# Kernel optimization log

Hardware: AMD Instinct MI355X
Metric: run time of the kernel (lower is better)

Reference implementation:

```python
import jax, jax.numpy as jnp
import numpy as np

N = 100000      # nodes
E = 1600000     # edges (before self-loops)
IN = 128        # in_size
H = 4           # heads
C = 32          # out_size // heads
OUT = H * C     # 128
NEG_SLOPE = 0.2
LN_EPS = 1e-5
SM_EPS = 1e-16  # PyG softmax eps


def setup_inputs() -> dict:
    key = jax.random.key(0)
    ks = jax.random.split(key, 6)
    x = jax.random.normal(ks[0], (N, IN), dtype=jnp.float32)
    edge_index = jax.random.randint(ks[1], (2, E), 0, N, dtype=jnp.int64)
    W = jax.random.normal(ks[2], (IN, OUT), dtype=jnp.float32) * 0.05
    a_src = jax.random.normal(ks[3], (H, C), dtype=jnp.float32) * 0.05
    a_dst = jax.random.normal(ks[4], (H, C), dtype=jnp.float32) * 0.05
    bias = jnp.zeros((OUT,), dtype=jnp.float32)
    gamma = jnp.ones((OUT,), dtype=jnp.float32)
    beta = jnp.zeros((OUT,), dtype=jnp.float32)
    return {"x": x, "edge_index": edge_index, "W": W, "a_src": a_src,
            "a_dst": a_dst, "bias": bias, "gamma": gamma, "beta": beta}


def reference(x, edge_index, W, a_src, a_dst, bias, gamma, beta):
    n = x.shape[0]
    # add self loops (PyG GATConv default)
    loops = jnp.arange(n, dtype=edge_index.dtype)
    src = jnp.concatenate([edge_index[0], loops])  # [E+N]
    dst = jnp.concatenate([edge_index[1], loops])

    h = (x @ W).reshape(n, H, C)                   # [N,H,C]
    alpha_src = jnp.sum(h * a_src, axis=-1)        # [N,H]
    alpha_dst = jnp.sum(h * a_dst, axis=-1)        # [N,H]

    e = jax.nn.leaky_relu(alpha_src[src] + alpha_dst[dst], NEG_SLOPE)  # [E+N,H]
    # segment softmax over edges grouped by destination node
    emax = jax.ops.segment_max(e, dst, num_segments=n)
    emax = jnp.where(jnp.isfinite(emax), emax, 0.0)
    ee = jnp.exp(e - emax[dst])
    denom = jax.ops.segment_sum(ee, dst, num_segments=n)
    alpha = ee / (denom[dst] + SM_EPS)             # [E+N,H]

    msg = h[src] * alpha[:, :, None]               # [E+N,H,C]
    out = jax.ops.segment_sum(msg, dst, num_segments=n).reshape(n, OUT) + bias

    # LayerNorm(out_size)
    mu = jnp.mean(out, axis=-1, keepdims=True)
    var = jnp.var(out, axis=-1, keepdims=True)
    out = (out - mu) * jax.lax.rsqrt(var + LN_EPS) * gamma + beta
    return jax.nn.relu(out)
```

## Files before the change

### kernel.cpp

```cpp
#include <hip/hip_runtime.h>
#include <hip/hip_bf16.h>
#include <math.h>

#define IN_DIM 128
#define OUT_DIM 128
#define NHEAD 4
#define HC 32
#define NEG_SLOPE 0.2f
#define LN_EPS 1e-5f
#define SM_EPS 1e-16f

#define NB_SHIFT 9
#define BDST 512
#define NBUCK_MAX 256
#define BIN_ITER 28
#define BIN_CHUNK (BIN_ITER * 256)
#define SRC_BITS 17
#define SRC_MASK ((1u << SRC_BITS) - 1u)

typedef __attribute__((ext_vector_type(8))) short bf16x8;
typedef __attribute__((ext_vector_type(4))) short short4v;
typedef __attribute__((ext_vector_type(4))) float f32x4;

__device__ __forceinline__ float leaky(float v) { return v > 0.f ? v : NEG_SLOPE * v; }

__device__ __forceinline__ short f2b(float f) {
    __hip_bfloat16 b = __float2bfloat16(f);
    return *reinterpret_cast<short*>(&b);
}

__device__ __forceinline__ int swz(int row, int byteInRow) {
    return row * 256 + (byteInRow ^ ((row & 7) << 4));
}

__global__ void k_prep(const float* __restrict__ W, __hip_bfloat16* __restrict__ WtB,
                       const int* __restrict__ ei, int* __restrict__ bcnt, int E, int N)
{
    int t0 = blockIdx.x * 256 + threadIdx.x;
    if (t0 < IN_DIM * OUT_DIM) {
        int k = t0 >> 7, j = t0 & 127;
        WtB[j * IN_DIM + k] = __float2bfloat16(W[t0]);
    }
    __shared__ int h[NBUCK_MAX];
    for (int i = threadIdx.x; i < NBUCK_MAX; i += blockDim.x) h[i] = 0;
    __syncthreads();
    int tot = E + N;
    for (int e = blockIdx.x * blockDim.x + threadIdx.x; e < tot; e += gridDim.x * blockDim.x) {
        int d = (e < E) ? ei[E + e] : (e - E);
        atomicAdd(&h[d >> NB_SHIFT], 1);
    }
    __syncthreads();
    for (int i = threadIdx.x; i < NBUCK_MAX; i += blockDim.x)
        if (h[i]) atomicAdd(&bcnt[i], h[i]);
}

__global__ void __launch_bounds__(256)
k_gemm_bin(const float* __restrict__ x, const __hip_bfloat16* __restrict__ WtB,
           const float* __restrict__ a_src, const float* __restrict__ a_dst,
           __hip_bfloat16* __restrict__ hB, float* __restrict__ asrc_out,
           float* __restrict__ adst_out,
           const int* __restrict__ ei, const int* __restrict__ bcnt,
           int* __restrict__ bcur, unsigned* __restrict__ binned,
           int E, int N, int nblk_gemm)
{
    __shared__ __align__(16) char lds[49152];
    const int t = threadIdx.x;

    if ((int)blockIdx.x < nblk_gemm) {
        const int node0 = blockIdx.x * 64;

        #pragma unroll
        for (int i = 0; i < 16; ++i) {
            int idx = (i * 256 + t) * 4;
            int col = idx >> 7, k = idx & 127;
            short4v w4 = *reinterpret_cast<const short4v*>((const short*)WtB + idx);
            *reinterpret_cast<short4v*>(lds + 16384 + swz(col, 2 * k)) = w4;
        }
        #pragma unroll
        for (int i = 0; i < 8; ++i) {
            int idx = (i * 256 + t) * 4;
            int row = idx >> 7, k = idx & 127;
            int node = node0 + row;
            float4 xv = make_float4(0.f, 0.f, 0.f, 0.f);
            if (node < N) xv = *reinterpret_cast<const float4*>(x + (size_t)node * IN_DIM + k);
            short4v xb = { f2b(xv.x), f2b(xv.y), f2b(xv.z), f2b(xv.w) };
            *reinterpret_cast<short4v*>(lds + swz(row, 2 * k)) = xb;
        }
        __syncthreads();

        const int wave = t >> 6, l = t & 63;
        const int lr = l & 15, lg = l >> 4;

        bf16x8 afrag[4];
        #pragma unroll
        for (int kk = 0; kk < 4; ++kk)
            afrag[kk] = *reinterpret_cast<bf16x8*>(lds + swz(wave * 16 + lr, kk * 64 + lg * 16));

        f32x4 acc[8];
        #pragma unroll
        for (int cg = 0; cg < 8; ++cg) acc[cg] = (f32x4){0.f, 0.f, 0.f, 0.f};

        #pragma unroll
        for (int cg = 0; cg < 8; ++cg) {
            #pragma unroll
            for (int kk = 0; kk < 4; ++kk) {
                bf16x8 b = *reinterpret_cast<bf16x8*>(lds + 16384 + swz(cg * 16 + lr, kk * 64 + lg * 16));
                acc[cg] = __builtin_amdgcn_mfma_f32_16x16x32_bf16(afrag[kk], b, acc[cg], 0, 0, 0);
            }
        }

        #pragma unroll
        for (int q = 0; q < 4; ++q) {
            int node = node0 + wave * 16 + lg * 4 + q;
            if (node < N) {
                #pragma unroll
                for (int cg = 0; cg < 8; ++cg)
                    hB[(size_t)node * OUT_DIM + cg * 16 + lr] = __float2bfloat16(acc[cg][q]);
            }
        }

        #pragma unroll
        for (int q = 0; q < 4; ++q) {
            int node = node0 + wave * 16 + lg * 4 + q;
            #pragma unroll
            for (int hh = 0; hh < 4; ++hh) {
                float as0 = a_src[hh * HC + lr], as1 = a_src[hh * HC + 16 + lr];
                float ad0 = a_dst[hh * HC + lr], ad1 = a_dst[hh * HC + 16 + lr];
                float s = acc[2 * hh][q] * as0 + acc[2 * hh + 1][q] * as1;
                float d = acc[2 * hh][q] * ad0 + acc[2 * hh + 1][q] * ad1;
                #pragma unroll
                for (int m = 1; m < 16; m <<= 1) {
                    s += __shfl_xor(s, m, 64);
                    d += __shfl_xor(d, m, 64);
                }
                if (lr == 0 && node < N) {
                    asrc_out[node * NHEAD + hh] = s;
                    adst_out[node * NHEAD + hh] = d;
                }
            }
        }
    } else {
        int* cnt = (int*)lds;
        int* gb  = (int*)(lds + 1024);
        int* sc  = (int*)(lds + 2048);
        int tot = E + N;
        int base = ((int)blockIdx.x - nblk_gemm) * BIN_CHUNK;

        int bv = bcnt[t];
        sc[t] = bv;
        __syncthreads();
        #pragma unroll
        for (int off = 1; off < NBUCK_MAX; off <<= 1) {
            int tmp = (t >= off) ? sc[t - off] : 0;
            __syncthreads();
            sc[t] += tmp;
            __syncthreads();
        }
        int bbase_t = sc[t] - bv;
        cnt[t] = 0;
        __syncthreads();

        int rk[BIN_ITER], bk[BIN_ITER], dlo[BIN_ITER];
        #pragma unroll
        for (int k = 0; k < BIN_ITER; ++k) {
            int e = base + k * 256 + t;
            bk[k] = -1; rk[k] = 0; dlo[k] = 0;
            if (e < tot) {
                int d = (e < E) ? ei[E + e] : (e - E);
                bk[k] = d >> NB_SHIFT;
                dlo[k] = d & (BDST - 1);
                rk[k] = atomicAdd(&cnt[bk[k]], 1);
            }
        }
        __syncthreads();
        gb[t] = cnt[t] ? (bbase_t + atomicAdd(&bcur[t], cnt[t])) : 0;
        __syncthreads();
        #pragma unroll
        for (int k = 0; k < BIN_ITER; ++k) {
            int e = base + k * 256 + t;
            if (e < tot) {
                int s = (e < E) ? ei[e] : (e - E);
                binned[gb[bk[k]] + rk[k]] = (unsigned)s | ((unsigned)dlo[k] << SRC_BITS);
            }
        }
    }
}

__global__ void k_bucket_csr(const unsigned* __restrict__ binned, const int* __restrict__ bcnt,
                             int* __restrict__ rowptr, int* __restrict__ csr_src,
                             int N, int tot, int nbuck)
{
    __shared__ int cnt[BDST];
    __shared__ int s2[256];
    int b = blockIdx.x;
    int t = threadIdx.x;
    int d0 = b << NB_SHIFT;

    int bv = bcnt[t];
    s2[t] = bv;
    __syncthreads();
    #pragma unroll
    for (int off = 1; off < NBUCK_MAX; off <<= 1) {
        int tmp = (t >= off) ? s2[t - off] : 0;
        __syncthreads();
        s2[t] += tmp;
        __syncthreads();
    }
    __shared__ int ebase_s, ne_s;
    if (t == b) { ebase_s = s2[t] - bv; ne_s = bv; }
    __syncthreads();
    int ebase = ebase_s, ne = ne_s;

    cnt[t] = 0; cnt[t + 256] = 0;
    __syncthreads();
    for (int i = t; i < ne; i += 256) {
        unsigned p = binned[ebase + i];
        atomicAdd(&cnt[p >> SRC_BITS], 1);
    }
    __syncthreads();
    int c0 = cnt[2 * t], c1 = cnt[2 * t + 1];
    s2[t] = c0 + c1;
    __syncthreads();
    #pragma unroll
    for (int off = 1; off < 256; off <<= 1) {
        int tmp = (t >= off) ? s2[t - off] : 0;
        __syncthreads();
        s2[t] += tmp;
        __syncthreads();
    }
    int e0 = (t ? s2[t - 1] : 0);
    cnt[2 * t] = e0;
    cnt[2 * t + 1] = e0 + c0;
    if (d0 + 2 * t < N)     rowptr[d0 + 2 * t]     = ebase + e0;
    if (d0 + 2 * t + 1 < N) rowptr[d0 + 2 * t + 1] = ebase + e0 + c0;
    if (b == nbuck - 1 && t == 0) rowptr[N] = tot;
    __syncthreads();
    for (int i = t; i < ne; i += 256) {
        unsigned p = binned[ebase + i];
        int r = atomicAdd(&cnt[p >> SRC_BITS], 1);
        csr_src[ebase + r] = (int)(p & SRC_MASK);
    }
}

__global__ void k_gather(const int* __restrict__ csr_src, const int* __restrict__ rowptr,
                         const __hip_bfloat16* __restrict__ hB,
                         const float* __restrict__ asrc, const float* __restrict__ adst,
                         const float* __restrict__ bias, const float* __restrict__ gamma,
                         const float* __restrict__ beta, float* __restrict__ out, int N)
{
    int wave = threadIdx.x >> 6;
    int l = threadIdx.x & 63;
    int d = blockIdx.x * 4 + wave;
    if (d >= N) return;
    int head = l >> 4;
    const char* hp = (const char*)hB;
    unsigned voff = (unsigned)(l << 2);
    float ad = adst[d * NHEAD + head];
    int beg = __builtin_amdgcn_readfirstlane(rowptr[d]);
    int end = __builtin_amdgcn_readfirstlane(rowptr[d + 1]);

    float ax0 = 0.f, ay0 = 0.f, dn0 = 0.f;
    float ax1 = 0.f, ay1 = 0.f, dn1 = 0.f;

    for (int c = beg; c < end; c += 16) {
        int rem = __builtin_amdgcn_readfirstlane(end - c);
        int idx = c + (l & 15);
        int cl = idx < end ? idx : end - 1;
        int smine = csr_src[cl];
        float v = (idx < end) ? asrc[(unsigned)smine * NHEAD + head] : -1e30f;
        float ee = __expf(leaky(v + ad));

#define GRP(E0_, E1_, E2_, E3_) {                                                     \
        unsigned s0_ = (unsigned)__builtin_amdgcn_readlane(smine, (E0_));             \
        unsigned s1_ = (unsigned)__builtin_amdgcn_readlane(smine, (E1_));             \
        unsigned s2_ = (unsigned)__builtin_amdgcn_readlane(smine, (E2_));             \
        unsigned s3_ = (unsigned)__builtin_amdgcn_readlane(smine, (E3_));             \
        unsigned hv0_ = *(const unsigned*)(hp + ((size_t)s0_ << 8) + voff);           \
        unsigned hv1_ = *(const unsigned*)(hp + ((size_t)s1_ << 8) + voff);           \
        unsigned hv2_ = *(const unsigned*)(hp + ((size_t)s2_ << 8) + voff);           \
        unsigned hv3_ = *(const unsigned*)(hp + ((size_t)s3_ << 8) + voff);           \
        float e0_ = __int_as_float(__builtin_amdgcn_ds_swizzle(                       \
            __float_as_int(ee), 0x10 | ((E0_) << 5)));                                \
        float e1_ = __int_as_float(__builtin_amdgcn_ds_swizzle(                       \
            __float_as_int(ee), 0x10 | ((E1_) << 5)));                                \
        float e2_ = __int_as_float(__builtin_amdgcn_ds_swizzle(                       \
            __float_as_int(ee), 0x10 | ((E2_) << 5)));                                \
        float e3_ = __int_as_float(__builtin_amdgcn_ds_swizzle(                       \
            __float_as_int(ee), 0x10 | ((E3_) << 5)));                                \
        ax0 = fmaf(e0_, __uint_as_float(hv0_ << 16), ax0);                            \
        ay0 = fmaf(e0_, __uint_as_float(hv0_ & 0xffff0000u), ay0);  dn0 += e0_;       \
        ax1 = fmaf(e1_, __uint_as_float(hv1_ << 16), ax1);                            \
        ay1 = fmaf(e1_, __uint_as_float(hv1_ & 0xffff0000u), ay1);  dn1 += e1_;       \
        ax0 = fmaf(e2_, __uint_as_float(hv2_ << 16), ax0);                            \
        ay0 = fmaf(e2_, __uint_as_float(hv2_ & 0xffff0000u), ay0);  dn0 += e2_;       \
        ax1 = fmaf(e3_, __uint_as_float(hv3_ << 16), ax1);                            \
        ay1 = fmaf(e3_, __uint_as_float(hv3_ & 0xffff0000u), ay1);  dn1 += e3_;       \
    }
        GRP(0, 1, 2, 3)
        if (rem > 4)  GRP(4, 5, 6, 7)
        if (rem > 8)  GRP(8, 9, 10, 11)
        if (rem > 12) GRP(12, 13, 14, 15)
#undef GRP
    }

    float accx = ax0 + ax1, accy = ay0 + ay1, den = dn0 + dn1;
    float inv = 1.f / (den + SM_EPS);
    float vx = accx * inv + bias[2 * l];
    float vy = accy * inv + bias[2 * l + 1];

    float s1 = vx + vy;
    float s2 = vx * vx + vy * vy;
    #pragma unroll
    for (int m = 32; m >= 1; m >>= 1) {
        s1 += __shfl_xor(s1, m, 64);
        s2 += __shfl_xor(s2, m, 64);
    }
    float mean = s1 * (1.f / OUT_DIM);
    float var = s2 * (1.f / OUT_DIM) - mean * mean;
    float r = rsqrtf(var + LN_EPS);
    float ox = (vx - mean) * r * gamma[2 * l] + beta[2 * l];
    float oy = (vy - mean) * r * gamma[2 * l + 1] + beta[2 * l + 1];
    ox = ox > 0.f ? ox : 0.f;
    oy = oy > 0.f ? oy : 0.f;
    *reinterpret_cast<float2*>(&out[(size_t)d * OUT_DIM + 2 * l]) = make_float2(ox, oy);
}

extern "C" void kernel_launch(void* const* d_in, const int* in_sizes, int n_in,
                              void* d_out, int out_size, void* d_ws, size_t ws_size,
                              hipStream_t stream) {
    const float* x      = (const float*)d_in[0];
    const int*   ei     = (const int*)d_in[1];
    const float* W      = (const float*)d_in[2];
    const float* a_src  = (const float*)d_in[3];
    const float* a_dst  = (const float*)d_in[4];
    const float* bias   = (const float*)d_in[5];
    const float* gamma  = (const float*)d_in[6];
    const float* beta   = (const float*)d_in[7];
    float* out = (float*)d_out;

    const int N = in_sizes[0] / IN_DIM;
    const int E = in_sizes[1] / 2;
    const int TOT = E + N;
    const int nbuck = (N + BDST - 1) >> NB_SHIFT;
    const int nblk_gemm = (N + 63) / 64;
    const int nblk_bin = (TOT + BIN_CHUNK - 1) / BIN_CHUNK;

    char* p = (char*)d_ws;
    __hip_bfloat16* hB = (__hip_bfloat16*)p;  p += (size_t)N * OUT_DIM * sizeof(__hip_bfloat16);
    __hip_bfloat16* WtB = (__hip_bfloat16*)p; p += (size_t)IN_DIM * OUT_DIM * sizeof(__hip_bfloat16);
    float* asrc   = (float*)p;                p += (size_t)N * NHEAD * sizeof(float);
    float* adst   = (float*)p;                p += (size_t)N * NHEAD * sizeof(float);
    int* bcnt     = (int*)p;                  p += NBUCK_MAX * sizeof(int);
    int* bcur     = (int*)p;                  p += NBUCK_MAX * sizeof(int);
    int* rowptr   = (int*)p;                  p += (size_t)(N + 1) * sizeof(int);
    unsigned* binned = (unsigned*)p;          p += (size_t)TOT * sizeof(unsigned);
    int* csr_src  = (int*)p;                  p += (size_t)TOT * sizeof(int);

    (void)hipMemsetAsync(bcnt, 0, 2 * NBUCK_MAX * sizeof(int), stream);

    k_prep<<<256, 256, 0, stream>>>(W, WtB, ei, bcnt, E, N);
    k_gemm_bin<<<nblk_gemm + nblk_bin, 256, 0, stream>>>(x, WtB, a_src, a_dst, hB, asrc, adst,
                                                         ei, bcnt, bcur, binned, E, N, nblk_gemm);
    k_bucket_csr<<<nbuck, 256, 0, stream>>>(binned, bcnt, rowptr, csr_src, N, TOT, nbuck);
    k_gather<<<(N + 3) / 4, 256, 0, stream>>>(csr_src, rowptr, hB, asrc, adst,
                                              bias, gamma, beta, out, N);
}
```

Baseline: 176.6 us.

## Use fixed-capacity buckets to drop histogram pass and prefetch gather indices

```diff
diff --git a/kernel.cpp b/kernel.cpp
--- a/kernel.cpp
+++ b/kernel.cpp
@@ -17,6 +17,8 @@
 #define BIN_CHUNK (BIN_ITER * 256)
 #define SRC_BITS 17
 #define SRC_MASK ((1u << SRC_BITS) - 1u)
+#define BCAP_SHIFT 14
+#define BCAP (1 << BCAP_SHIFT)
 
 typedef __attribute__((ext_vector_type(8))) short bf16x8;
 typedef __attribute__((ext_vector_type(4))) short short4v;
@@ -33,25 +35,11 @@
     return row * 256 + (byteInRow ^ ((row & 7) << 4));
 }
 
-__global__ void k_prep(const float* __restrict__ W, __hip_bfloat16* __restrict__ WtB,
-                       const int* __restrict__ ei, int* __restrict__ bcnt, int E, int N)
+__global__ void k_prepW(const float* __restrict__ W, __hip_bfloat16* __restrict__ WtB)
 {
     int t0 = blockIdx.x * 256 + threadIdx.x;
-    if (t0 < IN_DIM * OUT_DIM) {
-        int k = t0 >> 7, j = t0 & 127;
-        WtB[j * IN_DIM + k] = __float2bfloat16(W[t0]);
-    }
-    __shared__ int h[NBUCK_MAX];
-    for (int i = threadIdx.x; i < NBUCK_MAX; i += blockDim.x) h[i] = 0;
-    __syncthreads();
-    int tot = E + N;
-    for (int e = blockIdx.x * blockDim.x + threadIdx.x; e < tot; e += gridDim.x * blockDim.x) {
-        int d = (e < E) ? ei[E + e] : (e - E);
-        atomicAdd(&h[d >> NB_SHIFT], 1);
-    }
-    __syncthreads();
-    for (int i = threadIdx.x; i < NBUCK_MAX; i += blockDim.x)
-        if (h[i]) atomicAdd(&bcnt[i], h[i]);
+    int k = t0 >> 7, j = t0 & 127;
+    WtB[j * IN_DIM + k] = __float2bfloat16(W[t0]);
 }
 
 __global__ void __launch_bounds__(256)
@@ -59,8 +47,8 @@
            const float* __restrict__ a_src, const float* __restrict__ a_dst,
            __hip_bfloat16* __restrict__ hB, float* __restrict__ asrc_out,
            float* __restrict__ adst_out,
-           const int* __restrict__ ei, const int* __restrict__ bcnt,
-           int* __restrict__ bcur, unsigned* __restrict__ binned,
+           const int* __restrict__ ei, int* __restrict__ bcur,
+           unsigned* __restrict__ binned,
            int E, int N, int nblk_gemm)
 {
     __shared__ __align__(16) char lds[49152];
@@ -142,21 +130,9 @@
     } else {
         int* cnt = (int*)lds;
         int* gb  = (int*)(lds + 1024);
-        int* sc  = (int*)(lds + 2048);
         int tot = E + N;
         int base = ((int)blockIdx.x - nblk_gemm) * BIN_CHUNK;
 
-        int bv = bcnt[t];
-        sc[t] = bv;
-        __syncthreads();
-        #pragma unroll
-        for (int off = 1; off < NBUCK_MAX; off <<= 1) {
-            int tmp = (t >= off) ? sc[t - off] : 0;
-            __syncthreads();
-            sc[t] += tmp;
-            __syncthreads();
-        }
-        int bbase_t = sc[t] - bv;
         cnt[t] = 0;
         __syncthreads();
 
@@ -173,7 +149,7 @@
             }
         }
         __syncthreads();
-        gb[t] = cnt[t] ? (bbase_t + atomicAdd(&bcur[t], cnt[t])) : 0;
+        gb[t] = cnt[t] ? ((t << BCAP_SHIFT) + atomicAdd(&bcur[t], cnt[t])) : 0;
         __syncthreads();
         #pragma unroll
         for (int k = 0; k < BIN_ITER; ++k) {
@@ -186,35 +162,22 @@
     }
 }
 
-__global__ void k_bucket_csr(const unsigned* __restrict__ binned, const int* __restrict__ bcnt,
-                             int* __restrict__ rowptr, int* __restrict__ csr_src,
-                             int N, int tot, int nbuck)
+__global__ void k_bucket_csr(const unsigned* __restrict__ binned, const int* __restrict__ bcur,
+                             int* __restrict__ rowbeg, int* __restrict__ rowend,
+                             int* __restrict__ csr_src, int N)
 {
     __shared__ int cnt[BDST];
     __shared__ int s2[256];
     int b = blockIdx.x;
     int t = threadIdx.x;
     int d0 = b << NB_SHIFT;
-
-    int bv = bcnt[t];
-    s2[t] = bv;
-    __syncthreads();
-    #pragma unroll
-    for (int off = 1; off < NBUCK_MAX; off <<= 1) {
-        int tmp = (t >= off) ? s2[t - off] : 0;
-        __syncthreads();
-        s2[t] += tmp;
-        __syncthreads();
-    }
-    __shared__ int ebase_s, ne_s;
-    if (t == b) { ebase_s = s2[t] - bv; ne_s = bv; }
-    __syncthreads();
-    int ebase = ebase_s, ne = ne_s;
+    int base = b << BCAP_SHIFT;
+    int ne = bcur[b];
 
     cnt[t] = 0; cnt[t + 256] = 0;
     __syncthreads();
     for (int i = t; i < ne; i += 256) {
-        unsigned p = binned[ebase + i];
+        unsigned p = binned[base + i];
         atomicAdd(&cnt[p >> SRC_BITS], 1);
     }
     __syncthreads();
@@ -231,18 +194,24 @@
     int e0 = (t ? s2[t - 1] : 0);
     cnt[2 * t] = e0;
     cnt[2 * t + 1] = e0 + c0;
-    if (d0 + 2 * t < N)     rowptr[d0 + 2 * t]     = ebase + e0;
-    if (d0 + 2 * t + 1 < N) rowptr[d0 + 2 * t + 1] = ebase + e0 + c0;
-    if (b == nbuck - 1 && t == 0) rowptr[N] = tot;
+    if (d0 + 2 * t < N) {
+        rowbeg[d0 + 2 * t] = base + e0;
+        rowend[d0 + 2 * t] = base + e0 + c0;
+    }
+    if (d0 + 2 * t + 1 < N) {
+        rowbeg[d0 + 2 * t + 1] = base + e0 + c0;
+        rowend[d0 + 2 * t + 1] = base + e0 + c0 + c1;
+    }
     __syncthreads();
     for (int i = t; i < ne; i += 256) {
-        unsigned p = binned[ebase + i];
+        unsigned p = binned[base + i];
         int r = atomicAdd(&cnt[p >> SRC_BITS], 1);
-        csr_src[ebase + r] = (int)(p & SRC_MASK);
-    }
-}
-
-__global__ void k_gather(const int* __restrict__ csr_src, const int* __restrict__ rowptr,
+        csr_src[base + r] = (int)(p & SRC_MASK);
+    }
+}
+
+__global__ void k_gather(const int* __restrict__ csr_src,
+                         const int* __restrict__ rowbeg, const int* __restrict__ rowend,
                          const __hip_bfloat16* __restrict__ hB,
                          const float* __restrict__ asrc, const float* __restrict__ adst,
                          const float* __restrict__ bias, const float* __restrict__ gamma,
@@ -256,51 +225,49 @@
     const char* hp = (const char*)hB;
     unsigned voff = (unsigned)(l << 2);
     float ad = adst[d * NHEAD + head];
-    int beg = __builtin_amdgcn_readfirstlane(rowptr[d]);
-    int end = __builtin_amdgcn_readfirstlane(rowptr[d + 1]);
+    int beg = __builtin_amdgcn_readfirstlane(rowbeg[d]);
+    int end = __builtin_amdgcn_readfirstlane(rowend[d]);
 
     float ax0 = 0.f, ay0 = 0.f, dn0 = 0.f;
     float ax1 = 0.f, ay1 = 0.f, dn1 = 0.f;
 
+    int idx = beg + (l & 15);
+    int cl = idx < end ? idx : end - 1;
+    int smine = csr_src[cl];
+    float v = (idx < end) ? asrc[(unsigned)smine * NHEAD + head] : -1e30f;
+
     for (int c = beg; c < end; c += 16) {
-        int rem = __builtin_amdgcn_readfirstlane(end - c);
-        int idx = c + (l & 15);
-        int cl = idx < end ? idx : end - 1;
-        int smine = csr_src[cl];
-        float v = (idx < end) ? asrc[(unsigned)smine * NHEAD + head] : -1e30f;
         float ee = __expf(leaky(v + ad));
-
-#define GRP(E0_, E1_, E2_, E3_) {                                                     \
-        unsigned s0_ = (unsigned)__builtin_amdgcn_readlane(smine, (E0_));             \
-        unsigned s1_ = (unsigned)__builtin_amdgcn_readlane(smine, (E1_));             \
-        unsigned s2_ = (unsigned)__builtin_amdgcn_readlane(smine, (E2_));             \
-        unsigned s3_ = (unsigned)__builtin_amdgcn_readlane(smine, (E3_));             \
-        unsigned hv0_ = *(const unsigned*)(hp + ((size_t)s0_ << 8) + voff);           \
-        unsigned hv1_ = *(const unsigned*)(hp + ((size_t)s1_ << 8) + voff);           \
-        unsigned hv2_ = *(const unsigned*)(hp + ((size_t)s2_ << 8) + voff);           \
-        unsigned hv3_ = *(const unsigned*)(hp + ((size_t)s3_ << 8) + voff);           \
-        float e0_ = __int_as_float(__builtin_amdgcn_ds_swizzle(                       \
-            __float_as_int(ee), 0x10 | ((E0_) << 5)));                                \
-        float e1_ = __int_as_float(__builtin_amdgcn_ds_swizzle(                       \
-            __float_as_int(ee), 0x10 | ((E1_) << 5)));                                \
-        float e2_ = __int_as_float(__builtin_amdgcn_ds_swizzle(                       \
-            __float_as_int(ee), 0x10 | ((E2_) << 5)));                                \
-        float e3_ = __int_as_float(__builtin_amdgcn_ds_swizzle(                       \
-            __float_as_int(ee), 0x10 | ((E3_) << 5)));                                \
-        ax0 = fmaf(e0_, __uint_as_float(hv0_ << 16), ax0);                            \
-        ay0 = fmaf(e0_, __uint_as_float(hv0_ & 0xffff0000u), ay0);  dn0 += e0_;       \
-        ax1 = fmaf(e1_, __uint_as_float(hv1_ << 16), ax1);                            \
-        ay1 = fmaf(e1_, __uint_as_float(hv1_ & 0xffff0000u), ay1);  dn1 += e1_;       \
-        ax0 = fmaf(e2_, __uint_as_float(hv2_ << 16), ax0);                            \
-        ay0 = fmaf(e2_, __uint_as_float(hv2_ & 0xffff0000u), ay0);  dn0 += e2_;       \
-        ax1 = fmaf(e3_, __uint_as_float(hv3_ << 16), ax1);                            \
-        ay1 = fmaf(e3_, __uint_as_float(hv3_ & 0xffff0000u), ay1);  dn1 += e3_;       \
-    }
-        GRP(0, 1, 2, 3)
-        if (rem > 4)  GRP(4, 5, 6, 7)
-        if (rem > 8)  GRP(8, 9, 10, 11)
-        if (rem > 12) GRP(12, 13, 14, 15)
-#undef GRP
+        int scur = smine;
+        int c2 = c + 16;
+        if (c2 < end) {
+            int idx2 = c2 + (l & 15);
+            int cl2 = idx2 < end ? idx2 : end - 1;
+            smine = csr_src[cl2];
+            v = (idx2 < end) ? asrc[(unsigned)smine * NHEAD + head] : -1e30f;
+        }
+
+#define GLOAD(E_)                                                                     \
+        unsigned se##E_ = (unsigned)__builtin_amdgcn_readlane(scur, (E_));            \
+        unsigned hv##E_ = *(const unsigned*)(hp + ((size_t)se##E_ << 8) + voff);
+#define GCONS(E_, AX_, AY_, DN_) {                                                    \
+        float eb = __int_as_float(__builtin_amdgcn_ds_swizzle(                        \
+            __float_as_int(ee), 0x10 | ((E_) << 5)));                                 \
+        AX_ = fmaf(eb, __uint_as_float(hv##E_ << 16), AX_);                           \
+        AY_ = fmaf(eb, __uint_as_float(hv##E_ & 0xffff0000u), AY_);  DN_ += eb;       \
+    }
+        { GLOAD(0) GLOAD(1) GLOAD(2) GLOAD(3) GLOAD(4) GLOAD(5) GLOAD(6) GLOAD(7)
+          GCONS(0, ax0, ay0, dn0) GCONS(1, ax1, ay1, dn1)
+          GCONS(2, ax0, ay0, dn0) GCONS(3, ax1, ay1, dn1)
+          GCONS(4, ax0, ay0, dn0) GCONS(5, ax1, ay1, dn1)
+          GCONS(6, ax0, ay0, dn0) GCONS(7, ax1, ay1, dn1) }
+        { GLOAD(8) GLOAD(9) GLOAD(10) GLOAD(11) GLOAD(12) GLOAD(13) GLOAD(14) GLOAD(15)
+          GCONS(8, ax0, ay0, dn0)  GCONS(9, ax1, ay1, dn1)
+          GCONS(10, ax0, ay0, dn0) GCONS(11, ax1, ay1, dn1)
+          GCONS(12, ax0, ay0, dn0) GCONS(13, ax1, ay1, dn1)
+          GCONS(14, ax0, ay0, dn0) GCONS(15, ax1, ay1, dn1) }
+#undef GLOAD
+#undef GCONS
     }
 
     float accx = ax0 + ax1, accy = ay0 + ay1, den = dn0 + dn1;
@@ -350,18 +317,18 @@
     __hip_bfloat16* WtB = (__hip_bfloat16*)p; p += (size_t)IN_DIM * OUT_DIM * sizeof(__hip_bfloat16);
     float* asrc   = (float*)p;                p += (size_t)N * NHEAD * sizeof(float);
     float* adst   = (float*)p;                p += (size_t)N * NHEAD * sizeof(float);
-    int* bcnt     = (int*)p;                  p += NBUCK_MAX * sizeof(int);
     int* bcur     = (int*)p;                  p += NBUCK_MAX * sizeof(int);
-    int* rowptr   = (int*)p;                  p += (size_t)(N + 1) * sizeof(int);
-    unsigned* binned = (unsigned*)p;          p += (size_t)TOT * sizeof(unsigned);
-    int* csr_src  = (int*)p;                  p += (size_t)TOT * sizeof(int);
-
-    (void)hipMemsetAsync(bcnt, 0, 2 * NBUCK_MAX * sizeof(int), stream);
-
-    k_prep<<<256, 256, 0, stream>>>(W, WtB, ei, bcnt, E, N);
+    int* rowbeg   = (int*)p;                  p += (size_t)N * sizeof(int);
+    int* rowend   = (int*)p;                  p += (size_t)N * sizeof(int);
+    unsigned* binned = (unsigned*)p;          p += (size_t)nbuck * BCAP * sizeof(unsigned);
+    int* csr_src  = (int*)p;                  p += (size_t)nbuck * BCAP * sizeof(int);
+
+    (void)hipMemsetAsync(bcur, 0, NBUCK_MAX * sizeof(int), stream);
+
+    k_prepW<<<64, 256, 0, stream>>>(W, WtB);
     k_gemm_bin<<<nblk_gemm + nblk_bin, 256, 0, stream>>>(x, WtB, a_src, a_dst, hB, asrc, adst,
-                                                         ei, bcnt, bcur, binned, E, N, nblk_gemm);
-    k_bucket_csr<<<nbuck, 256, 0, stream>>>(binned, bcnt, rowptr, csr_src, N, TOT, nbuck);
-    k_gather<<<(N + 3) / 4, 256, 0, stream>>>(csr_src, rowptr, hB, asrc, adst,
+                                                         ei, bcur, binned, E, N, nblk_gemm);
+    k_bucket_csr<<<nbuck, 256, 0, stream>>>(binned, bcur, rowbeg, rowend, csr_src, N);
+    k_gather<<<(N + 3) / 4, 256, 0, stream>>>(csr_src, rowbeg, rowend, hB, asrc, adst,
                                               bias, gamma, beta, out, N);
 }
```

Measured after the change: 161.6 us. 1.09x faster.
